# Optimization experiments

Measured on AMD Instinct MI355X. Metric: run time of the kernel, lower is better.

Reference implementation:

```python
import jax, jax.numpy as jnp
import numpy as np

DICE_W = 0.5
CHAMFER_W = 0.5
SMOOTH = 1e-6


def setup_inputs() -> dict:
    key = jax.random.key(0)
    k1, k2, k3, k4 = jax.random.split(key, 4)
    B, H, W = 4, 1024, 1024
    N = M = 8192
    predictions = jax.random.normal(k1, (B, 1, H, W), dtype=jnp.float32)   # logits
    target = jax.random.uniform(k2, (B, 1, H, W), dtype=jnp.float32)       # soft GT mask
    pred_points = jax.random.normal(k3, (1, N, 2), dtype=jnp.float32)      # pred boundary pts
    target_points = jax.random.normal(k4, (1, M, 2), dtype=jnp.float32)    # GT boundary pts
    return {"predictions": predictions, "target": target,
            "pred_points": pred_points, "target_points": target_points}


def _dice_loss(pred_logits, target):
    pred = jax.nn.sigmoid(pred_logits)
    intersection = jnp.sum(pred * target)
    union = jnp.sum(pred) + jnp.sum(target)
    dice = (2.0 * intersection + SMOOTH) / (union + SMOOTH)
    return 1.0 - dice


def _chamfer_loss(pred_points, target_points):
    # pairwise squared distances: (1, N, M)
    diff = pred_points[:, :, None, :] - target_points[:, None, :, :]
    d2 = jnp.sum(diff * diff, axis=-1)
    # bidirectional chamfer: mean of nearest-neighbor sq-dist in each direction
    return jnp.mean(jnp.min(d2, axis=2)) + jnp.mean(jnp.min(d2, axis=1))


def reference(predictions, target, pred_points, target_points):
    dice = _dice_loss(predictions, target)
    chamfer = _chamfer_loss(pred_points, target_points)
    return DICE_W * dice + CHAMFER_W * chamfer
```

## Files before the change

### kernel.cpp

```cpp
#include <hip/hip_runtime.h>
#include <math.h>

#define INFBITS 0x7F800000u
#define TCH 128
#define PTS 8
#define DICE_BLOCKS 512

__device__ __forceinline__ float block_sum256(float v) {
#pragma unroll
    for (int o = 32; o > 0; o >>= 1) v += __shfl_down(v, o, 64);
    __shared__ float sb[4];
    if ((threadIdx.x & 63) == 0) sb[threadIdx.x >> 6] = v;
    __syncthreads();
    float r = sb[0] + sb[1] + sb[2] + sb[3];
    __syncthreads();
    return r;
}

__global__ void __launch_bounds__(256) fused_partials(
        const float4* __restrict__ p4, const float4* __restrict__ t4, int n4,
        float* __restrict__ inter_p, float* __restrict__ uni_p,
        const float2* __restrict__ P, const float2* __restrict__ T,
        int N, int M, float* __restrict__ pm, int npm, int chm, int gxp,
        unsigned int* __restrict__ counter) {
    int bid = blockIdx.x;
    if (bid == 0 && threadIdx.x == 0) *counter = 0u;

    if (bid < DICE_BLOCKS) {
        float inter = 0.f, uni = 0.f;
#pragma unroll 2
        for (int i = bid * 256 + threadIdx.x; i < n4; i += DICE_BLOCKS * 256) {
            float4 p = p4[i];
            float4 t = t4[i];
            float s;
            s = __fdividef(1.f, 1.f + __expf(-p.x)); inter = fmaf(s, t.x, inter); uni += s + t.x;
            s = __fdividef(1.f, 1.f + __expf(-p.y)); inter = fmaf(s, t.y, inter); uni += s + t.y;
            s = __fdividef(1.f, 1.f + __expf(-p.z)); inter = fmaf(s, t.z, inter); uni += s + t.z;
            s = __fdividef(1.f, 1.f + __expf(-p.w)); inter = fmaf(s, t.w, inter); uni += s + t.w;
        }
        float bi = block_sum256(inter);
        float bu = block_sum256(uni);
        if (threadIdx.x == 0) { inter_p[bid] = bi; uni_p[bid] = bu; }
        return;
    }

    int cb      = bid - DICE_BLOCKS;
    int per_dir = gxp * chm;
    int dir     = cb / per_dir;
    int rem     = cb - dir * per_dir;
    int cy      = rem / gxp;
    int cx      = rem - cy * gxp;
    const float2* A = dir ? T : P;
    const float2* B = dir ? P : T;
    int nA = dir ? M : N;
    int nB = dir ? N : M;

    int tb = cy * TCH;
    if (tb >= nB) return;

    __shared__ __align__(16) float2 xy[TCH];
    int t = threadIdx.x;
    if (t < TCH) {
        float2 b = make_float2(1e18f, 1e18f);
        if (tb + t < nB) b = B[tb + t];
        xy[t] = b;
    }
    __syncthreads();

    int abase = cx * (PTS * 256);
    float nx[PTS], ny[PTS], mn[PTS];
#pragma unroll
    for (int i = 0; i < PTS; ++i) {
        int p = abase + i * 256 + t;
        nx[i] = 0.f; ny[i] = 0.f;
        mn[i] = __uint_as_float(INFBITS);
        if (p < nA) {
            float2 a = A[p];
            nx[i] = -2.f * a.x;
            ny[i] = -2.f * a.y;
        }
    }

#pragma unroll 4
    for (int j = 0; j < TCH; j += 2) {
        float4 q = *(const float4*)&xy[j];
        float s20 = fmaf(q.x, q.x, q.y * q.y);
        float s21 = fmaf(q.z, q.z, q.w * q.w);
#pragma unroll
        for (int i = 0; i < PTS; ++i)
            mn[i] = fminf(mn[i], fmaf(nx[i], q.x, fmaf(ny[i], q.y, s20)));
#pragma unroll
        for (int i = 0; i < PTS; ++i)
            mn[i] = fminf(mn[i], fmaf(nx[i], q.z, fmaf(ny[i], q.w, s21)));
    }

    float* dstc = pm + ((size_t)dir * chm + cy) * npm;
#pragma unroll
    for (int i = 0; i < PTS; ++i) {
        int p = abase + i * 256 + t;
        if (p < nA) dstc[p] = mn[i];
    }
}

__global__ void __launch_bounds__(256) finalize_all(
        const float* __restrict__ pm, int npm, int chm,
        int N, int M, int nch0, int nch1,
        const float2* __restrict__ P, const float2* __restrict__ T,
        const float* __restrict__ inter_p, const float* __restrict__ uni_p,
        float* __restrict__ bsum, unsigned int* __restrict__ counter,
        int gxf, float* __restrict__ out) {
    int blk = blockIdx.x;
    int dir = blk / gxf;
    int bx  = blk - dir * gxf;
    int nA  = dir ? M : N;
    int nch = dir ? nch1 : nch0;
    const float2* A = dir ? T : P;

    int p = bx * 256 + threadIdx.x;
    float v = 0.f;
    if (p < nA) {
        const float* src = pm + (size_t)dir * chm * npm + p;
        float m = __uint_as_float(INFBITS);
#pragma unroll 16
        for (int c = 0; c < nch; ++c) m = fminf(m, src[(size_t)c * npm]);
        float2 a = A[p];
        v = m + fmaf(a.x, a.x, a.y * a.y);
    }
    float s = block_sum256(v);

    __shared__ int is_last;
    if (threadIdx.x == 0) {
        bsum[blk] = s;
        __threadfence();
        unsigned int old = atomicAdd(counter, 1u);
        is_last = (old == (unsigned)(2 * gxf - 1));
    }
    __syncthreads();
    if (!is_last) return;
    __threadfence();

    float inter = 0.f, uni = 0.f, c0 = 0.f, c1 = 0.f;
    for (int i = threadIdx.x; i < DICE_BLOCKS; i += 256) {
        inter += inter_p[i];
        uni   += uni_p[i];
    }
    const volatile float* vb = bsum;
    for (int i = threadIdx.x; i < gxf; i += 256) {
        c0 += vb[i];
        c1 += vb[gxf + i];
    }
    float bi  = block_sum256(inter);
    float bu  = block_sum256(uni);
    float bc0 = block_sum256(c0);
    float bc1 = block_sum256(c1);
    if (threadIdx.x == 0) {
        const float SMOOTH = 1e-6f;
        float dice    = (2.f * bi + SMOOTH) / (bu + SMOOTH);
        float chamfer = bc0 / (float)N + bc1 / (float)M;
        out[0] = 0.5f * (1.f - dice) + 0.5f * chamfer;
    }
}

extern "C" void kernel_launch(void* const* d_in, const int* in_sizes, int n_in,
                              void* d_out, int out_size, void* d_ws, size_t ws_size,
                              hipStream_t stream) {
    const float*  pred = (const float*)d_in[0];
    const float*  targ = (const float*)d_in[1];
    const float2* pp   = (const float2*)d_in[2];
    const float2* tp   = (const float2*)d_in[3];
    int n = in_sizes[0];
    int N = in_sizes[2] / 2;
    int M = in_sizes[3] / 2;
    float* out = (float*)d_out;

    int npm  = N > M ? N : M;
    int nch0 = (M + TCH - 1) / TCH;
    int nch1 = (N + TCH - 1) / TCH;
    int chm  = nch0 > nch1 ? nch0 : nch1;
    int gxp  = (npm + PTS * 256 - 1) / (PTS * 256);
    int gxf  = (npm + 255) / 256;

    char*  ws      = (char*)d_ws;
    float* pm      = (float*)ws;
    size_t pm_bytes = (size_t)2 * chm * npm * sizeof(float);
    size_t off     = (pm_bytes + 255) & ~(size_t)255;
    float* inter_p = (float*)(ws + off);
    float* uni_p   = inter_p + DICE_BLOCKS;
    float* bsum    = uni_p + DICE_BLOCKS;
    unsigned int* counter = (unsigned int*)(bsum + 2 * gxf);

    int cham_blocks = 2 * gxp * chm;
    fused_partials<<<DICE_BLOCKS + cham_blocks, 256, 0, stream>>>(
        (const float4*)pred, (const float4*)targ, n / 4,
        inter_p, uni_p, pp, tp, N, M, pm, npm, chm, gxp, counter);

    finalize_all<<<2 * gxf, 256, 0, stream>>>(pm, npm, chm, N, M, nch0, nch1,
                                              pp, tp, inter_p, uni_p, bsum,
                                              counter, gxf, out);
}
```

Baseline: 28.71 us.

## Merge chamfer reduction into one kernel via atomicMin and last-block finalize

Drops the per-chunk partial-min buffer and the separate finalize kernel. Each chamfer block now atomicMins its nearest-neighbour squared distances, stored as float bits, into per-point arrays that a memset fills with all-ones bits before launch. The counter is also preset by that memset, so the last block to finish sums the per-point minima and the dice partials and writes the loss. This trades a large partial-buffer write and reread, plus a second launch, for about a million global atomics, an extra memset and a serial single-block tail that reads all points.

New measurement: 79.84 us. +178.1%, slower.

```diff
diff --git a/kernel.cpp b/kernel.cpp
--- a/kernel.cpp
+++ b/kernel.cpp
@@ -17,143 +17,119 @@
     return r;
 }
 
-__global__ void __launch_bounds__(256) fused_partials(
+__global__ void __launch_bounds__(256) fused_all(
         const float4* __restrict__ p4, const float4* __restrict__ t4, int n4,
         float* __restrict__ inter_p, float* __restrict__ uni_p,
         const float2* __restrict__ P, const float2* __restrict__ T,
-        int N, int M, float* __restrict__ pm, int npm, int chm, int gxp,
-        unsigned int* __restrict__ counter) {
+        int N, int M,
+        unsigned int* __restrict__ m0, unsigned int* __restrict__ m1,
+        unsigned int* __restrict__ counter,
+        int chm, int gxp, int nblk, float* __restrict__ out) {
     int bid = blockIdx.x;
-    if (bid == 0 && threadIdx.x == 0) *counter = 0u;
+    int t   = threadIdx.x;
 
     if (bid < DICE_BLOCKS) {
         float inter = 0.f, uni = 0.f;
 #pragma unroll 2
-        for (int i = bid * 256 + threadIdx.x; i < n4; i += DICE_BLOCKS * 256) {
+        for (int i = bid * 256 + t; i < n4; i += DICE_BLOCKS * 256) {
             float4 p = p4[i];
-            float4 t = t4[i];
+            float4 tt = t4[i];
             float s;
-            s = __fdividef(1.f, 1.f + __expf(-p.x)); inter = fmaf(s, t.x, inter); uni += s + t.x;
-            s = __fdividef(1.f, 1.f + __expf(-p.y)); inter = fmaf(s, t.y, inter); uni += s + t.y;
-            s = __fdividef(1.f, 1.f + __expf(-p.z)); inter = fmaf(s, t.z, inter); uni += s + t.z;
-            s = __fdividef(1.f, 1.f + __expf(-p.w)); inter = fmaf(s, t.w, inter); uni += s + t.w;
+            s = __fdividef(1.f, 1.f + __expf(-p.x)); inter = fmaf(s, tt.x, inter); uni += s + tt.x;
+            s = __fdividef(1.f, 1.f + __expf(-p.y)); inter = fmaf(s, tt.y, inter); uni += s + tt.y;
+            s = __fdividef(1.f, 1.f + __expf(-p.z)); inter = fmaf(s, tt.z, inter); uni += s + tt.z;
+            s = __fdividef(1.f, 1.f + __expf(-p.w)); inter = fmaf(s, tt.w, inter); uni += s + tt.w;
         }
         float bi = block_sum256(inter);
         float bu = block_sum256(uni);
-        if (threadIdx.x == 0) { inter_p[bid] = bi; uni_p[bid] = bu; }
-        return;
-    }
+        if (t == 0) { inter_p[bid] = bi; uni_p[bid] = bu; }
+    } else {
+        int cb      = bid - DICE_BLOCKS;
+        int per_dir = gxp * chm;
+        int dir     = cb / per_dir;
+        int rem     = cb - dir * per_dir;
+        int cy      = rem / gxp;
+        int cx      = rem - cy * gxp;
+        const float2* A = dir ? T : P;
+        const float2* B = dir ? P : T;
+        int nA = dir ? M : N;
+        int nB = dir ? N : M;
+        unsigned int* marr = dir ? m1 : m0;
 
-    int cb      = bid - DICE_BLOCKS;
-    int per_dir = gxp * chm;
-    int dir     = cb / per_dir;
-    int rem     = cb - dir * per_dir;
-    int cy      = rem / gxp;
-    int cx      = rem - cy * gxp;
-    const float2* A = dir ? T : P;
-    const float2* B = dir ? P : T;
-    int nA = dir ? M : N;
-    int nB = dir ? N : M;
+        int tb = cy * TCH;
+        if (tb < nB) {
+            __shared__ __align__(16) float2 xy[TCH];
+            if (t < TCH) {
+                float2 b = make_float2(1e18f, 1e18f);
+                if (tb + t < nB) b = B[tb + t];
+                xy[t] = b;
+            }
+            __syncthreads();
 
-    int tb = cy * TCH;
-    if (tb >= nB) return;
+            int abase = cx * (PTS * 256);
+            float nx[PTS], ny[PTS], mn[PTS];
+#pragma unroll
+            for (int i = 0; i < PTS; ++i) {
+                int p = abase + i * 256 + t;
+                nx[i] = 0.f; ny[i] = 0.f;
+                mn[i] = __uint_as_float(INFBITS);
+                if (p < nA) {
+                    float2 a = A[p];
+                    nx[i] = -2.f * a.x;
+                    ny[i] = -2.f * a.y;
+                }
+            }
 
-    __shared__ __align__(16) float2 xy[TCH];
-    int t = threadIdx.x;
-    if (t < TCH) {
-        float2 b = make_float2(1e18f, 1e18f);
-        if (tb + t < nB) b = B[tb + t];
-        xy[t] = b;
-    }
-    __syncthreads();
+#pragma unroll 4
+            for (int j = 0; j < TCH; j += 2) {
+                float4 q = *(const float4*)&xy[j];
+                float s20 = fmaf(q.x, q.x, q.y * q.y);
+                float s21 = fmaf(q.z, q.z, q.w * q.w);
+#pragma unroll
+                for (int i = 0; i < PTS; ++i)
+                    mn[i] = fminf(mn[i], fmaf(nx[i], q.x, fmaf(ny[i], q.y, s20)));
+#pragma unroll
+                for (int i = 0; i < PTS; ++i)
+                    mn[i] = fminf(mn[i], fmaf(nx[i], q.z, fmaf(ny[i], q.w, s21)));
+            }
 
-    int abase = cx * (PTS * 256);
-    float nx[PTS], ny[PTS], mn[PTS];
 #pragma unroll
-    for (int i = 0; i < PTS; ++i) {
-        int p = abase + i * 256 + t;
-        nx[i] = 0.f; ny[i] = 0.f;
-        mn[i] = __uint_as_float(INFBITS);
-        if (p < nA) {
-            float2 a = A[p];
-            nx[i] = -2.f * a.x;
-            ny[i] = -2.f * a.y;
+            for (int i = 0; i < PTS; ++i) {
+                int p = abase + i * 256 + t;
+                if (p < nA) {
+                    float sa  = 0.25f * fmaf(nx[i], nx[i], ny[i] * ny[i]);
+                    float key = fmaxf(mn[i] + sa, 0.f);
+                    atomicMin(marr + p, __float_as_uint(key));
+                }
+            }
+            __threadfence();
         }
     }
 
-#pragma unroll 4
-    for (int j = 0; j < TCH; j += 2) {
-        float4 q = *(const float4*)&xy[j];
-        float s20 = fmaf(q.x, q.x, q.y * q.y);
-        float s21 = fmaf(q.z, q.z, q.w * q.w);
-#pragma unroll
-        for (int i = 0; i < PTS; ++i)
-            mn[i] = fminf(mn[i], fmaf(nx[i], q.x, fmaf(ny[i], q.y, s20)));
-#pragma unroll
-        for (int i = 0; i < PTS; ++i)
-            mn[i] = fminf(mn[i], fmaf(nx[i], q.z, fmaf(ny[i], q.w, s21)));
-    }
-
-    float* dstc = pm + ((size_t)dir * chm + cy) * npm;
-#pragma unroll
-    for (int i = 0; i < PTS; ++i) {
-        int p = abase + i * 256 + t;
-        if (p < nA) dstc[p] = mn[i];
-    }
-}
-
-__global__ void __launch_bounds__(256) finalize_all(
-        const float* __restrict__ pm, int npm, int chm,
-        int N, int M, int nch0, int nch1,
-        const float2* __restrict__ P, const float2* __restrict__ T,
-        const float* __restrict__ inter_p, const float* __restrict__ uni_p,
-        float* __restrict__ bsum, unsigned int* __restrict__ counter,
-        int gxf, float* __restrict__ out) {
-    int blk = blockIdx.x;
-    int dir = blk / gxf;
-    int bx  = blk - dir * gxf;
-    int nA  = dir ? M : N;
-    int nch = dir ? nch1 : nch0;
-    const float2* A = dir ? T : P;
-
-    int p = bx * 256 + threadIdx.x;
-    float v = 0.f;
-    if (p < nA) {
-        const float* src = pm + (size_t)dir * chm * npm + p;
-        float m = __uint_as_float(INFBITS);
-#pragma unroll 16
-        for (int c = 0; c < nch; ++c) m = fminf(m, src[(size_t)c * npm]);
-        float2 a = A[p];
-        v = m + fmaf(a.x, a.x, a.y * a.y);
-    }
-    float s = block_sum256(v);
-
+    __syncthreads();
     __shared__ int is_last;
-    if (threadIdx.x == 0) {
-        bsum[blk] = s;
+    if (t == 0) {
         __threadfence();
         unsigned int old = atomicAdd(counter, 1u);
-        is_last = (old == (unsigned)(2 * gxf - 1));
+        is_last = (old == (unsigned)(nblk - 2));
     }
     __syncthreads();
     if (!is_last) return;
-    __threadfence();
 
-    float inter = 0.f, uni = 0.f, c0 = 0.f, c1 = 0.f;
-    for (int i = threadIdx.x; i < DICE_BLOCKS; i += 256) {
-        inter += inter_p[i];
-        uni   += uni_p[i];
-    }
-    const volatile float* vb = bsum;
-    for (int i = threadIdx.x; i < gxf; i += 256) {
-        c0 += vb[i];
-        c1 += vb[gxf + i];
-    }
+    float c0 = 0.f, c1 = 0.f, inter = 0.f, uni = 0.f;
+    for (int i = t; i < N; i += 256)
+        c0 += __uint_as_float(atomicMin(m0 + i, 0xFFFFFFFFu));
+    for (int i = t; i < M; i += 256)
+        c1 += __uint_as_float(atomicMin(m1 + i, 0xFFFFFFFFu));
+    const volatile float* vi = inter_p;
+    const volatile float* vu = uni_p;
+    for (int i = t; i < DICE_BLOCKS; i += 256) { inter += vi[i]; uni += vu[i]; }
+
     float bi  = block_sum256(inter);
     float bu  = block_sum256(uni);
     float bc0 = block_sum256(c0);
     float bc1 = block_sum256(c1);
-    if (threadIdx.x == 0) {
+    if (t == 0) {
         const float SMOOTH = 1e-6f;
         float dice    = (2.f * bi + SMOOTH) / (bu + SMOOTH);
         float chamfer = bc0 / (float)N + bc1 / (float)M;
@@ -173,28 +149,25 @@
     int M = in_sizes[3] / 2;
     float* out = (float*)d_out;
 
-    int npm  = N > M ? N : M;
-    int nch0 = (M + TCH - 1) / TCH;
-    int nch1 = (N + TCH - 1) / TCH;
-    int chm  = nch0 > nch1 ? nch0 : nch1;
-    int gxp  = (npm + PTS * 256 - 1) / (PTS * 256);
-    int gxf  = (npm + 255) / 256;
+    int npm = N > M ? N : M;
+    int chm = (npm + TCH - 1) / TCH;
+    int gxp = (npm + PTS * 256 - 1) / (PTS * 256);
+    int cham_blocks = 2 * gxp * chm;
+    int nblk = DICE_BLOCKS + cham_blocks;
 
-    char*  ws      = (char*)d_ws;
-    float* pm      = (float*)ws;
-    size_t pm_bytes = (size_t)2 * chm * npm * sizeof(float);
-    size_t off     = (pm_bytes + 255) & ~(size_t)255;
+    char* ws = (char*)d_ws;
+    unsigned int* m0      = (unsigned int*)ws;
+    unsigned int* m1      = m0 + N;
+    unsigned int* counter = m1 + M;
+    size_t msz = (size_t)(N + M + 1) * sizeof(unsigned int);
+    size_t off = (msz + 255) & ~(size_t)255;
     float* inter_p = (float*)(ws + off);
     float* uni_p   = inter_p + DICE_BLOCKS;
-    float* bsum    = uni_p + DICE_BLOCKS;
-    unsigned int* counter = (unsigned int*)(bsum + 2 * gxf);
 
-    int cham_blocks = 2 * gxp * chm;
-    fused_partials<<<DICE_BLOCKS + cham_blocks, 256, 0, stream>>>(
+    hipMemsetAsync(ws, 0xFF, msz, stream);
+
+    fused_all<<<nblk, 256, 0, stream>>>(
         (const float4*)pred, (const float4*)targ, n / 4,
-        inter_p, uni_p, pp, tp, N, M, pm, npm, chm, gxp, counter);
-
-    finalize_all<<<2 * gxf, 256, 0, stream>>>(pm, npm, chm, N, M, nch0, nch1,
-                                              pp, tp, inter_p, uni_p, bsum,
-                                              counter, gxf, out);
+        inter_p, uni_p, pp, tp, N, M, m0, m1, counter,
+        chm, gxp, nblk, out);
 }
```
